# Optimization experiments

Hardware: AMD Instinct MI355X
Metric: run time of the kernel (lower is better)

Reference implementation:

```python
import jax, jax.numpy as jnp
import numpy as np

NUM_HEAD = 16


def setup_inputs() -> dict:
    key = jax.random.key(0)
    ks = jax.random.split(key, 4)
    B, C, D = 2, 2048, 1024
    hidden_states = jax.random.normal(ks[0], (B, C, D), dtype=jnp.float32)
    attention_mask = jnp.zeros((B, 1, C, C), dtype=jnp.float32)
    Wqkv = jax.random.normal(ks[1], (D, 3 * D), dtype=jnp.float32) * (D ** -0.5)
    bqkv = jnp.zeros((3 * D,), dtype=jnp.float32)
    Wo = jax.random.normal(ks[2], (D, D), dtype=jnp.float32) * (D ** -0.5)
    bo = jnp.zeros((D,), dtype=jnp.float32)
    return {"hidden_states": hidden_states, "attention_mask": attention_mask,
            "Wqkv": Wqkv, "bqkv": bqkv, "Wo": Wo, "bo": bo}


def reference(hidden_states, attention_mask, Wqkv, bqkv, Wo, bo):
    B, C, D = hidden_states.shape
    H = NUM_HEAD
    hd = D // H
    scaling = hd ** -0.5

    qkv = hidden_states @ Wqkv + bqkv                      # [B, C, 3D]
    q, k, v = jnp.split(qkv, 3, axis=-1)
    # [B, C, H, hd] -> [B, H, C, hd]
    q = q.reshape(B, C, H, hd).transpose(0, 2, 1, 3)
    k = k.reshape(B, C, H, hd).transpose(0, 2, 1, 3)
    v = v.reshape(B, C, H, hd).transpose(0, 2, 1, 3)

    scores = jnp.einsum("bhqd,bhkd->bhqk", q, k) * scaling  # [B, H, C, C]
    causal = jnp.tril(jnp.ones((C, C), dtype=bool))[None, None]
    mask = jnp.where(causal, attention_mask, -jnp.inf)      # [B, 1, C, C]
    probs = jax.nn.softmax(scores + mask, axis=-1)
    out = jnp.einsum("bhqk,bhkd->bhqd", probs, v)           # [B, H, C, hd]
    out = out.transpose(0, 2, 1, 3).reshape(B, C, D)
    return out @ Wo + bo
```

## Files before the change

### kernel.cpp

```cpp
#include <hip/hip_runtime.h>
#include <hip/hip_bf16.h>
#include <cstdint>
#include <cstddef>

typedef __attribute__((ext_vector_type(8))) short short8;
typedef __attribute__((ext_vector_type(4))) float f32x4;
typedef unsigned short u16;
typedef unsigned int u32;

#define B_ 2
#define C_ 2048
#define D_ 1024
#define H_ 16
#define HD_ 64

static __device__ __forceinline__ u16 f2b(float f) {
  u32 x = __builtin_bit_cast(u32, f);
  x += 0x7FFFu + ((x >> 16) & 1u);
  return (u16)(x >> 16);
}

__global__ void k_convert(const float* __restrict__ in, u16* __restrict__ out, int n) {
  int i = (blockIdx.x * blockDim.x + threadIdx.x) * 4;
  const int stride = gridDim.x * blockDim.x * 4;
  for (; i < n; i += stride) {
    float4 v = *reinterpret_cast<const float4*>(in + i);
    ushort4 o;
    o.x = f2b(v.x); o.y = f2b(v.y); o.z = f2b(v.z); o.w = f2b(v.w);
    *reinterpret_cast<ushort4*>(out + i) = o;
  }
}

__global__ void k_tconv(const float* __restrict__ in, u16* __restrict__ out, int R, int Cc) {
  __shared__ float tile[64][65];
  const int tC = blockIdx.x * 64;
  const int tR = blockIdx.y * 64;
  const int t = threadIdx.x;
  const int r0 = t >> 4;
  const int c0 = (t & 15) * 4;
#pragma unroll
  for (int ii = 0; ii < 4; ++ii) {
    int r = ii * 16 + r0;
    float4 v = *reinterpret_cast<const float4*>(&in[(size_t)(tR + r) * Cc + tC + c0]);
    tile[r][c0] = v.x; tile[r][c0 + 1] = v.y; tile[r][c0 + 2] = v.z; tile[r][c0 + 3] = v.w;
  }
  __syncthreads();
#pragma unroll
  for (int ii = 0; ii < 4; ++ii) {
    int c = ii * 16 + r0;
    ushort4 o;
    o.x = f2b(tile[c0 + 0][c]);
    o.y = f2b(tile[c0 + 1][c]);
    o.z = f2b(tile[c0 + 2][c]);
    o.w = f2b(tile[c0 + 3][c]);
    *reinterpret_cast<ushort4*>(&out[(size_t)(tC + c) * R + tR + c0]) = o;
  }
}

__global__ void k_maskflags(const float* __restrict__ mask, u32* __restrict__ flags) {
  const int bid = blockIdx.x;
  const int kt = bid & 15, qt = (bid >> 4) & 31, b = bid >> 9;
  const int t = threadIdx.x;
  const float* base = mask + ((size_t)b * C_ + qt * 64) * C_ + kt * 128;
  const int row = t >> 2, c0 = (t & 3) * 32;
  int any = 0;
#pragma unroll
  for (int i = 0; i < 8; ++i) {
    float4 v = *reinterpret_cast<const float4*>(base + (size_t)row * C_ + c0 + i * 4);
    any |= (v.x != 0.f) | (v.y != 0.f) | (v.z != 0.f) | (v.w != 0.f);
  }
  __shared__ int sh[4];
  const unsigned long long bal = __ballot(any);
  if ((t & 63) == 0) sh[t >> 6] = (bal != 0ull);
  __syncthreads();
  if (t == 0) flags[bid] = (u32)(sh[0] | sh[1] | sh[2] | sh[3]);
}

#define GLL16(gptr, lptr) __builtin_amdgcn_global_load_lds( \
    (const __attribute__((address_space(1))) u32*)(gptr),   \
    (__attribute__((address_space(3))) u32*)(lptr), 16, 0, 0)

template<int EPI, int BM>
__global__ __launch_bounds__(256) void k_gemm(
    const u16* __restrict__ A, const u16* __restrict__ Bt,
    int M, int N, int K, const float* __restrict__ bias,
    u16* __restrict__ Cq, u16* __restrict__ Ck, u16* __restrict__ Cv,
    float* __restrict__ Cf)
{
  constexpr int WCW = (BM == 128) ? 64 : 32;
  constexpr int NF = WCW / 16;
  __shared__ __align__(16) u16 As[BM * 64];
  __shared__ __align__(16) u16 Bs[128 * 64];
  const int t = threadIdx.x;
  const int l = t & 63, w = t >> 6;
  const int wr = (BM == 128) ? (w >> 1) : 0;
  const int wc = (BM == 128) ? (w & 1) : w;
  const int lr = l & 15, lg = l >> 4;
  const int swk = lr & 7;
  const int m0 = blockIdx.y * BM, n0 = blockIdx.x * 128;
  f32x4 acc[4][NF] = {};

  for (int k0 = 0; k0 < K; k0 += 64) {
#pragma unroll
    for (int s = 0; s < BM / 32; ++s) {
      const int u = s * 256 + t;
      const int row = u >> 3, slot = (u & 7) ^ (row & 7);
      GLL16(A + (size_t)(m0 + row) * K + k0 + (slot << 3), As + (u << 3));
    }
#pragma unroll
    for (int s = 0; s < 4; ++s) {
      const int u = s * 256 + t;
      const int row = u >> 3, slot = (u & 7) ^ (row & 7);
      GLL16(Bt + (size_t)(n0 + row) * K + k0 + (slot << 3), Bs + (u << 3));
    }
    __syncthreads();
    short8 af[2][4], bfr[2][NF];
#pragma unroll
    for (int s = 0; s < 2; ++s) {
#pragma unroll
      for (int m = 0; m < 4; ++m)
        af[s][m] = *reinterpret_cast<const short8*>(
            &As[((wr * 64 + m * 16 + lr) << 6) + (((s * 4 + lg) ^ swk) << 3)]);
#pragma unroll
      for (int n = 0; n < NF; ++n)
        bfr[s][n] = *reinterpret_cast<const short8*>(
            &Bs[((wc * WCW + n * 16 + lr) << 6) + (((s * 4 + lg) ^ swk) << 3)]);
    }
#pragma unroll
    for (int s = 0; s < 2; ++s)
#pragma unroll
      for (int m = 0; m < 4; ++m)
#pragma unroll
        for (int n = 0; n < NF; ++n)
          acc[m][n] = __builtin_amdgcn_mfma_f32_16x16x32_bf16(af[s][m], bfr[s][n], acc[m][n], 0, 0, 0);
    __syncthreads();
  }

#pragma unroll
  for (int m = 0; m < 4; ++m) {
    const int mg = m0 + wr * 64 + m * 16 + lg * 4;
    const int bq = mg >> 11, c0 = mg & 2047;
#pragma unroll
    for (int n = 0; n < NF; ++n) {
      const int ng = n0 + wc * WCW + n * 16 + lr;
      const float bia = bias[ng];
      if (EPI == 0) {
        const int reg = ng >> 10, d = ng & 1023, h = d >> 6, e = d & 63;
        if (reg == 2) {
          u16* vp = Cv + (((size_t)(bq * H_ + h) * HD_ + e) << 11) + c0;
#pragma unroll
          for (int j = 0; j < 4; ++j) vp[j] = f2b(acc[m][n][j] + bia);
        } else {
          u16* dst = (reg == 0) ? Cq : Ck;
#pragma unroll
          for (int j = 0; j < 4; ++j)
            dst[(((size_t)(bq * H_ + h) * C_ + c0 + j) << 6) + e] = f2b(acc[m][n][j] + bia);
        }
      } else {
#pragma unroll
        for (int j = 0; j < 4; ++j)
          Cf[(size_t)(mg + j) * N + ng] = acc[m][n][j] + bia;
      }
    }
  }
}

static __device__ __forceinline__ void stage_kv(
    const u16* __restrict__ Kbh, const u16* __restrict__ Vbh,
    u16* Kd, u16* Vd, int kt, int t)
{
#pragma unroll
  for (int ch = 0; ch < 4; ++ch) {
    const int u = ch * 256 + t;
    const int krow = u >> 3, kslot = (u & 7) ^ (krow & 7);
    GLL16(Kbh + (((size_t)(kt * 128 + krow)) << 6) + (kslot << 3), Kd + (u << 3));
    const int vrow = u >> 4, vslot = (u & 15) ^ (vrow & 7);
    GLL16(Vbh + (((size_t)vrow) << 11) + kt * 128 + (vslot << 3), Vd + (u << 3));
  }
}

__global__ __launch_bounds__(256) void k_attn(
    const u16* __restrict__ Q, const u16* __restrict__ Kb, const u16* __restrict__ Vt,
    const float* __restrict__ mask, const u32* __restrict__ flags, u16* __restrict__ O)
{
  __shared__ __align__(16) u16 Kl[2][128 * 64];
  __shared__ __align__(16) u16 Vl[2][64 * 128];
  __shared__ __align__(16) u16 Pl[4][16 * 128];
  const int bid = blockIdx.x;
  const int bh = bid & 31;
  const int pair = bid >> 5;
  const int b = bh >> 4, h = bh & 15;
  const int t = threadIdx.x;
  const int l = t & 63, w = t >> 6;
  const int lr = l & 15, lg = l >> 4;
  const int swk = lr & 7;
  const float scaling = 0.125f;

  const u16* Kbh = Kb + (size_t)bh * C_ * HD_;
  const u16* Vbh = Vt + (size_t)bh * HD_ * C_;
  u16* Pw = Pl[w];

#pragma unroll 1
  for (int phase = 0; phase < 2; ++phase) {
    const int qt = phase ? (31 - pair) : pair;
    const int ktmax = qt >> 1;
    const int qrb = qt * 64 + w * 16 + lg * 4;

    short8 aq[2];
    {
      const int qrow = qt * 64 + w * 16 + lr;
      const u16* qp = Q + ((size_t)bh * C_ + qrow) * HD_ + lg * 8;
      aq[0] = *reinterpret_cast<const short8*>(qp);
      aq[1] = *reinterpret_cast<const short8*>(qp + 32);
    }
    float mrun[4], srun[4];
    f32x4 oacc[4] = {};
#pragma unroll
    for (int j = 0; j < 4; ++j) { mrun[j] = -INFINITY; srun[j] = 0.f; }
    const float* mbase = mask + ((size_t)b * C_ + qrb) * C_ + lr;
    const u32* fbase = flags + ((b << 5) + qt) * 16;

    __builtin_amdgcn_s_barrier();
    stage_kv(Kbh, Vbh, Kl[0], Vl[0], 0, t);

    for (int kt = 0; kt <= ktmax; ++kt) {
      const int cur = kt & 1;
      asm volatile("s_waitcnt vmcnt(0)" ::: "memory");
      __builtin_amdgcn_s_barrier();

      const u32 mflag = fbase[kt];

      f32x4 sf[8] = {};
      __builtin_amdgcn_s_setprio(1);
#pragma unroll
      for (int s = 0; s < 2; ++s)
#pragma unroll
        for (int nf = 0; nf < 8; ++nf) {
          const short8 bk = *reinterpret_cast<const short8*>(
              &Kl[cur][((nf * 16 + lr) << 6) + (((s * 4 + lg) ^ swk) << 3)]);
          sf[nf] = __builtin_amdgcn_mfma_f32_16x16x32_bf16(aq[s], bk, sf[nf], 0, 0, 0);
        }
      __builtin_amdgcn_s_setprio(0);

      if (kt < ktmax) stage_kv(Kbh, Vbh, Kl[cur ^ 1], Vl[cur ^ 1], kt + 1, t);

      if (mflag) {
#pragma unroll
        for (int nf = 0; nf < 8; ++nf)
#pragma unroll
          for (int j = 0; j < 4; ++j)
            sf[nf][j] = fmaf(sf[nf][j], scaling, mbase[(size_t)j * C_ + kt * 128 + nf * 16]);
      } else {
#pragma unroll
        for (int nf = 0; nf < 8; ++nf)
#pragma unroll
          for (int j = 0; j < 4; ++j)
            sf[nf][j] *= scaling;
      }
      if (kt == ktmax) {
#pragma unroll
        for (int nf = 0; nf < 8; ++nf) {
          const int key = kt * 128 + nf * 16 + lr;
#pragma unroll
          for (int j = 0; j < 4; ++j)
            if (key > qrb + j) sf[nf][j] = -INFINITY;
        }
      }

      float pm[4] = {-INFINITY, -INFINITY, -INFINITY, -INFINITY};
#pragma unroll
      for (int nf = 0; nf < 8; ++nf)
#pragma unroll
        for (int j = 0; j < 4; ++j) pm[j] = fmaxf(pm[j], sf[nf][j]);
#pragma unroll
      for (int j = 0; j < 4; ++j) {
        pm[j] = fmaxf(pm[j], __shfl_xor(pm[j], 1));
        pm[j] = fmaxf(pm[j], __shfl_xor(pm[j], 2));
        pm[j] = fmaxf(pm[j], __shfl_xor(pm[j], 4));
        pm[j] = fmaxf(pm[j], __shfl_xor(pm[j], 8));
      }
#pragma unroll
      for (int j = 0; j < 4; ++j) {
        const float mn = fmaxf(mrun[j], pm[j]);
        const float rescale = __expf(mrun[j] - mn);
        float rsum = 0.f;
#pragma unroll
        for (int nf = 0; nf < 8; ++nf) {
          const float e = __expf(sf[nf][j] - mn);
          sf[nf][j] = e;
          rsum += e;
        }
        rsum += __shfl_xor(rsum, 1);
        rsum += __shfl_xor(rsum, 2);
        rsum += __shfl_xor(rsum, 4);
        rsum += __shfl_xor(rsum, 8);
        srun[j] = srun[j] * rescale + rsum;
        mrun[j] = mn;
#pragma unroll
        for (int df = 0; df < 4; ++df) oacc[df][j] *= rescale;
      }

#pragma unroll
      for (int j = 0; j < 4; ++j) {
        const int prow = lg * 4 + j;
        const int psw = (prow & 7) << 3;
#pragma unroll
        for (int nf = 0; nf < 8; ++nf)
          Pw[(prow << 7) + ((nf * 16 + lr) ^ psw)] = f2b(sf[nf][j]);
      }

      __builtin_amdgcn_s_setprio(1);
#pragma unroll
      for (int s2 = 0; s2 < 4; ++s2) {
        const short8 ap = *reinterpret_cast<const short8*>(
            &Pw[(lr << 7) + (((s2 * 4 + lg) ^ swk) << 3)]);
#pragma unroll
        for (int df = 0; df < 4; ++df) {
          const short8 bv = *reinterpret_cast<const short8*>(
              &Vl[cur][((df * 16 + lr) << 7) + (((s2 * 4 + lg) ^ swk) << 3)]);
          oacc[df] = __builtin_amdgcn_mfma_f32_16x16x32_bf16(ap, bv, oacc[df], 0, 0, 0);
        }
      }
      __builtin_amdgcn_s_setprio(0);
    }

    float rinv[4];
#pragma unroll
    for (int j = 0; j < 4; ++j) rinv[j] = 1.f / srun[j];
#pragma unroll
    for (int df = 0; df < 4; ++df) {
      const int dcol = df * 16 + lr;
#pragma unroll
      for (int j = 0; j < 4; ++j)
        O[((size_t)b * C_ + qrb + j) * D_ + h * HD_ + dcol] = f2b(oacc[df][j] * rinv[j]);
    }
  }
}

extern "C" void kernel_launch(void* const* d_in, const int* in_sizes, int n_in,
                              void* d_out, int out_size, void* d_ws, size_t ws_size,
                              hipStream_t stream) {
  const float* hs   = (const float*)d_in[0];
  const float* mask = (const float*)d_in[1];
  const float* Wqkv = (const float*)d_in[2];
  const float* bqkv = (const float*)d_in[3];
  const float* Wo   = (const float*)d_in[4];
  const float* bo   = (const float*)d_in[5];
  float* out = (float*)d_out;
  char* ws = (char*)d_ws;

  u16* hsb   = (u16*)(ws);
  u16* Wqkvt = (u16*)(ws + (8  << 20));
  u16* Wot   = (u16*)(ws + (14 << 20));
  u16* Qb    = (u16*)(ws + (16 << 20));
  u16* Kb    = (u16*)(ws + (24 << 20));
  u32* flags = (u32*)(ws + (32 << 20));
  u16* Vtb   = (u16*)(ws + (40 << 20));
  u16* AOb   = (u16*)(ws + (48 << 20));

  k_convert<<<2048, 256, 0, stream>>>(hs, hsb, 4096 * 1024);
  k_tconv<<<dim3(3072 / 64, 1024 / 64), 256, 0, stream>>>(Wqkv, Wqkvt, 1024, 3072);
  k_tconv<<<dim3(1024 / 64, 1024 / 64), 256, 0, stream>>>(Wo, Wot, 1024, 1024);
  k_maskflags<<<1024, 256, 0, stream>>>(mask, flags);
  k_gemm<0, 128><<<dim3(24, 32), 256, 0, stream>>>(hsb, Wqkvt, 4096, 3072, 1024, bqkv,
                                                   Qb, Kb, Vtb, nullptr);
  k_attn<<<512, 256, 0, stream>>>(Qb, Kb, Vtb, mask, flags, AOb);
  k_gemm<1, 64><<<dim3(8, 64), 256, 0, stream>>>(AOb, Wot, 4096, 1024, 1024, bo,
                                                 nullptr, nullptr, nullptr, out);
}
```

Measured before the change: 154.0 us.

## Rewrite attention with 32x32x16 MFMA, 128-row query tiles and 64-key blocks

The attention kernel now gives each wave 32 query rows and computes S^T = K·Q^T and O^T with 32x32x16 bf16 MFMAs over 64-key tiles. This lets row softmax reductions use one cross-half shuffle instead of four. Q is prescaled by 1/8 on load, P is packed with v_cvt_pk_bf16_f32, and the output is staged through LDS for coalesced 16-byte stores. Mask flags are recomputed at 64x64 granularity to match the new tiling. The grid shrinks to 256 blocks, which reduces parallelism, and prescaling Q in bf16 adds extra rounding.

```diff
diff --git a/kernel.cpp b/kernel.cpp
--- a/kernel.cpp
+++ b/kernel.cpp
@@ -5,6 +5,7 @@
 
 typedef __attribute__((ext_vector_type(8))) short short8;
 typedef __attribute__((ext_vector_type(4))) float f32x4;
+typedef __attribute__((ext_vector_type(16))) float f32x16;
 typedef unsigned short u16;
 typedef unsigned int u32;
 
@@ -59,13 +60,13 @@
 
 __global__ void k_maskflags(const float* __restrict__ mask, u32* __restrict__ flags) {
   const int bid = blockIdx.x;
-  const int kt = bid & 15, qt = (bid >> 4) & 31, b = bid >> 9;
+  const int kt = bid & 31, qs = (bid >> 5) & 31, b = bid >> 10;
   const int t = threadIdx.x;
-  const float* base = mask + ((size_t)b * C_ + qt * 64) * C_ + kt * 128;
-  const int row = t >> 2, c0 = (t & 3) * 32;
+  const float* base = mask + ((size_t)b * C_ + qs * 64) * C_ + kt * 64;
+  const int row = t >> 2, c0 = (t & 3) * 16;
   int any = 0;
 #pragma unroll
-  for (int i = 0; i < 8; ++i) {
+  for (int i = 0; i < 4; ++i) {
     float4 v = *reinterpret_cast<const float4*>(base + (size_t)row * C_ + c0 + i * 4);
     any |= (v.x != 0.f) | (v.y != 0.f) | (v.z != 0.f) | (v.w != 0.f);
   }
@@ -170,12 +171,11 @@
     u16* Kd, u16* Vd, int kt, int t)
 {
 #pragma unroll
-  for (int ch = 0; ch < 4; ++ch) {
+  for (int ch = 0; ch < 2; ++ch) {
     const int u = ch * 256 + t;
-    const int krow = u >> 3, kslot = (u & 7) ^ (krow & 7);
-    GLL16(Kbh + (((size_t)(kt * 128 + krow)) << 6) + (kslot << 3), Kd + (u << 3));
-    const int vrow = u >> 4, vslot = (u & 15) ^ (vrow & 7);
-    GLL16(Vbh + (((size_t)vrow) << 11) + kt * 128 + (vslot << 3), Vd + (u << 3));
+    const int row = u >> 3, slot = (u & 7) ^ (row & 7);
+    GLL16(Kbh + (((size_t)(kt * 64 + row)) << 6) + (slot << 3), Kd + (u << 3));
+    GLL16(Vbh + (((size_t)row) << 11) + kt * 64 + (slot << 3), Vd + (u << 3));
   }
 }
 
@@ -183,156 +183,155 @@
     const u16* __restrict__ Q, const u16* __restrict__ Kb, const u16* __restrict__ Vt,
     const float* __restrict__ mask, const u32* __restrict__ flags, u16* __restrict__ O)
 {
-  __shared__ __align__(16) u16 Kl[2][128 * 64];
-  __shared__ __align__(16) u16 Vl[2][64 * 128];
-  __shared__ __align__(16) u16 Pl[4][16 * 128];
+  __shared__ __align__(16) u16 Kl[2][64 * 64];
+  __shared__ __align__(16) u16 Vl[2][64 * 64];
+  __shared__ __align__(16) u16 Sc[4][2304];
   const int bid = blockIdx.x;
   const int bh = bid & 31;
-  const int pair = bid >> 5;
+  const int pr = bid >> 5;
   const int b = bh >> 4, h = bh & 15;
   const int t = threadIdx.x;
   const int l = t & 63, w = t >> 6;
-  const int lr = l & 15, lg = l >> 4;
-  const int swk = lr & 7;
-  const float scaling = 0.125f;
-
-  const u16* Kbh = Kb + (size_t)bh * C_ * HD_;
-  const u16* Vbh = Vt + (size_t)bh * HD_ * C_;
-  u16* Pw = Pl[w];
+  const int q = l & 31, hi = l >> 5;
+  const int q7 = q & 7;
+
+  const u16* Kbh = Kb + (size_t)bh * (C_ * HD_);
+  const u16* Vbh = Vt + (size_t)bh * (HD_ * C_);
+  char* Swb = reinterpret_cast<char*>(Sc[w]);
 
 #pragma unroll 1
   for (int phase = 0; phase < 2; ++phase) {
-    const int qt = phase ? (31 - pair) : pair;
-    const int ktmax = qt >> 1;
-    const int qrb = qt * 64 + w * 16 + lg * 4;
-
-    short8 aq[2];
+    const int qt = phase ? (15 - pr) : pr;
+    const int ktb = 2 * qt + 2;
+    const int q0w = qt * 128 + w * 32;
+    const int qg = q0w + q;
+    const int qmaxw = q0w + 31;
+
+    short8 aq[4];
     {
-      const int qrow = qt * 64 + w * 16 + lr;
-      const u16* qp = Q + ((size_t)bh * C_ + qrow) * HD_ + lg * 8;
-      aq[0] = *reinterpret_cast<const short8*>(qp);
-      aq[1] = *reinterpret_cast<const short8*>(qp + 32);
-    }
-    float mrun[4], srun[4];
-    f32x4 oacc[4] = {};
-#pragma unroll
-    for (int j = 0; j < 4; ++j) { mrun[j] = -INFINITY; srun[j] = 0.f; }
-    const float* mbase = mask + ((size_t)b * C_ + qrb) * C_ + lr;
-    const u32* fbase = flags + ((b << 5) + qt) * 16;
-
-    __builtin_amdgcn_s_barrier();
+      const u16* qp = Q + ((size_t)bh * C_ + qg) * HD_ + hi * 8;
+#pragma unroll
+      for (int kh = 0; kh < 4; ++kh) {
+        short8 v = *reinterpret_cast<const short8*>(qp + kh * 16);
+#pragma unroll
+        for (int i = 0; i < 8; ++i) {
+          const float f = __builtin_bit_cast(float, (u32)((u16)v[i]) << 16) * 0.125f;
+          v[i] = (short)f2b(f);
+        }
+        aq[kh] = v;
+      }
+    }
+
+    f32x16 oa0 = {}, oa1 = {};
+    float mrun = -INFINITY, srun = 0.f;
+    const float* mrow = mask + ((size_t)b * C_ + qg) * C_;
+    const u32* fb = flags + (size_t)(b * 32 + (q0w >> 6)) * 32;
+
     stage_kv(Kbh, Vbh, Kl[0], Vl[0], 0, t);
 
-    for (int kt = 0; kt <= ktmax; ++kt) {
+#pragma unroll 1
+    for (int kt = 0; kt < ktb; ++kt) {
       const int cur = kt & 1;
-      asm volatile("s_waitcnt vmcnt(0)" ::: "memory");
-      __builtin_amdgcn_s_barrier();
-
-      const u32 mflag = fbase[kt];
-
-      f32x4 sf[8] = {};
-      __builtin_amdgcn_s_setprio(1);
-#pragma unroll
-      for (int s = 0; s < 2; ++s)
-#pragma unroll
-        for (int nf = 0; nf < 8; ++nf) {
-          const short8 bk = *reinterpret_cast<const short8*>(
-              &Kl[cur][((nf * 16 + lr) << 6) + (((s * 4 + lg) ^ swk) << 3)]);
-          sf[nf] = __builtin_amdgcn_mfma_f32_16x16x32_bf16(aq[s], bk, sf[nf], 0, 0, 0);
-        }
-      __builtin_amdgcn_s_setprio(0);
-
-      if (kt < ktmax) stage_kv(Kbh, Vbh, Kl[cur ^ 1], Vl[cur ^ 1], kt + 1, t);
-
-      if (mflag) {
-#pragma unroll
-        for (int nf = 0; nf < 8; ++nf)
-#pragma unroll
-          for (int j = 0; j < 4; ++j)
-            sf[nf][j] = fmaf(sf[nf][j], scaling, mbase[(size_t)j * C_ + kt * 128 + nf * 16]);
-      } else {
-#pragma unroll
-        for (int nf = 0; nf < 8; ++nf)
-#pragma unroll
-          for (int j = 0; j < 4; ++j)
-            sf[nf][j] *= scaling;
-      }
-      if (kt == ktmax) {
-#pragma unroll
-        for (int nf = 0; nf < 8; ++nf) {
-          const int key = kt * 128 + nf * 16 + lr;
-#pragma unroll
-          for (int j = 0; j < 4; ++j)
-            if (key > qrb + j) sf[nf][j] = -INFINITY;
-        }
-      }
-
-      float pm[4] = {-INFINITY, -INFINITY, -INFINITY, -INFINITY};
-#pragma unroll
-      for (int nf = 0; nf < 8; ++nf)
-#pragma unroll
-        for (int j = 0; j < 4; ++j) pm[j] = fmaxf(pm[j], sf[nf][j]);
-#pragma unroll
-      for (int j = 0; j < 4; ++j) {
-        pm[j] = fmaxf(pm[j], __shfl_xor(pm[j], 1));
-        pm[j] = fmaxf(pm[j], __shfl_xor(pm[j], 2));
-        pm[j] = fmaxf(pm[j], __shfl_xor(pm[j], 4));
-        pm[j] = fmaxf(pm[j], __shfl_xor(pm[j], 8));
-      }
-#pragma unroll
-      for (int j = 0; j < 4; ++j) {
-        const float mn = fmaxf(mrun[j], pm[j]);
-        const float rescale = __expf(mrun[j] - mn);
-        float rsum = 0.f;
-#pragma unroll
-        for (int nf = 0; nf < 8; ++nf) {
-          const float e = __expf(sf[nf][j] - mn);
-          sf[nf][j] = e;
-          rsum += e;
-        }
-        rsum += __shfl_xor(rsum, 1);
-        rsum += __shfl_xor(rsum, 2);
-        rsum += __shfl_xor(rsum, 4);
-        rsum += __shfl_xor(rsum, 8);
-        srun[j] = srun[j] * rescale + rsum;
-        mrun[j] = mn;
-#pragma unroll
-        for (int df = 0; df < 4; ++df) oacc[df][j] *= rescale;
-      }
-
-#pragma unroll
-      for (int j = 0; j < 4; ++j) {
-        const int prow = lg * 4 + j;
-        const int psw = (prow & 7) << 3;
-#pragma unroll
-        for (int nf = 0; nf < 8; ++nf)
-          Pw[(prow << 7) + ((nf * 16 + lr) ^ psw)] = f2b(sf[nf][j]);
-      }
-
-      __builtin_amdgcn_s_setprio(1);
-#pragma unroll
-      for (int s2 = 0; s2 < 4; ++s2) {
-        const short8 ap = *reinterpret_cast<const short8*>(
-            &Pw[(lr << 7) + (((s2 * 4 + lg) ^ swk) << 3)]);
-#pragma unroll
-        for (int df = 0; df < 4; ++df) {
-          const short8 bv = *reinterpret_cast<const short8*>(
-              &Vl[cur][((df * 16 + lr) << 7) + (((s2 * 4 + lg) ^ swk) << 3)]);
-          oacc[df] = __builtin_amdgcn_mfma_f32_16x16x32_bf16(ap, bv, oacc[df], 0, 0, 0);
-        }
-      }
-      __builtin_amdgcn_s_setprio(0);
-    }
-
-    float rinv[4];
-#pragma unroll
-    for (int j = 0; j < 4; ++j) rinv[j] = 1.f / srun[j];
-#pragma unroll
-    for (int df = 0; df < 4; ++df) {
-      const int dcol = df * 16 + lr;
-#pragma unroll
-      for (int j = 0; j < 4; ++j)
-        O[((size_t)b * C_ + qrb + j) * D_ + h * HD_ + dcol] = f2b(oacc[df][j] * rinv[j]);
+      __syncthreads();
+      if (kt + 1 < ktb) stage_kv(Kbh, Vbh, Kl[cur ^ 1], Vl[cur ^ 1], kt + 1, t);
+      if (kt * 64 > qmaxw) continue;
+
+      const char* Kc = reinterpret_cast<const char*>(Kl[cur]);
+      const char* Vc = reinterpret_cast<const char*>(Vl[cur]);
+
+      f32x16 p0 = {}, p1 = {};
+#pragma unroll
+      for (int kh = 0; kh < 4; ++kh) {
+        const int sl = ((2 * kh + hi) ^ q7) << 4;
+        const short8 k0 = *reinterpret_cast<const short8*>(Kc + q * 128 + sl);
+        const short8 k1 = *reinterpret_cast<const short8*>(Kc + (32 + q) * 128 + sl);
+        p0 = __builtin_amdgcn_mfma_f32_32x32x16_bf16(k0, aq[kh], p0, 0, 0, 0);
+        p1 = __builtin_amdgcn_mfma_f32_32x32x16_bf16(k1, aq[kh], p1, 0, 0, 0);
+      }
+
+      if (fb[kt]) {
+        const float* mp = mrow + kt * 64 + 4 * hi;
+#pragma unroll
+        for (int g = 0; g < 4; ++g) {
+          const float4 m0 = *reinterpret_cast<const float4*>(mp + 8 * g);
+          const float4 m1 = *reinterpret_cast<const float4*>(mp + 32 + 8 * g);
+          p0[4*g+0] += m0.x; p0[4*g+1] += m0.y; p0[4*g+2] += m0.z; p0[4*g+3] += m0.w;
+          p1[4*g+0] += m1.x; p1[4*g+1] += m1.y; p1[4*g+2] += m1.z; p1[4*g+3] += m1.w;
+        }
+      }
+      if (kt * 64 + 63 > q0w) {
+#pragma unroll
+        for (int r = 0; r < 16; ++r) {
+          const int kl = kt * 64 + (r & 3) + 8 * (r >> 2) + 4 * hi;
+          if (kl > qg) p0[r] = -INFINITY;
+          if (kl + 32 > qg) p1[r] = -INFINITY;
+        }
+      }
+
+      float pm = -INFINITY;
+#pragma unroll
+      for (int r = 0; r < 16; ++r) pm = fmaxf(pm, fmaxf(p0[r], p1[r]));
+      pm = fmaxf(pm, __shfl_xor(pm, 32));
+      const float mn = fmaxf(fmaxf(mrun, pm), -1e30f);
+      const float rs = __expf(mrun - mn);
+      float sum = 0.f;
+#pragma unroll
+      for (int r = 0; r < 16; ++r) {
+        p0[r] = __expf(p0[r] - mn); sum += p0[r];
+        p1[r] = __expf(p1[r] - mn); sum += p1[r];
+      }
+      sum += __shfl_xor(sum, 32);
+      srun = srun * rs + sum;
+      mrun = mn;
+      oa0 *= rs; oa1 *= rs;
+
+#pragma unroll
+      for (int g = 0; g < 4; ++g) {
+#pragma unroll
+        for (int m = 0; m < 2; ++m) {
+          u32 w0, w1;
+          asm("v_cvt_pk_bf16_f32 %0, %1, %2" : "=v"(w0) : "v"(p0[4*g+2*m]), "v"(p0[4*g+2*m+1]));
+          asm("v_cvt_pk_bf16_f32 %0, %1, %2" : "=v"(w1) : "v"(p1[4*g+2*m]), "v"(p1[4*g+2*m+1]));
+          *reinterpret_cast<u32*>(Swb + q * 128 + ((g ^ q7) << 4) + 8 * hi + 4 * m) = w0;
+          *reinterpret_cast<u32*>(Swb + q * 128 + (((4 + g) ^ q7) << 4) + 8 * hi + 4 * m) = w1;
+        }
+      }
+      asm volatile("" ::: "memory");
+
+#pragma unroll
+      for (int ks = 0; ks < 4; ++ks) {
+        const int sl = ((2 * ks + hi) ^ q7) << 4;
+        const short8 bp = *reinterpret_cast<const short8*>(Swb + q * 128 + sl);
+        const short8 v0 = *reinterpret_cast<const short8*>(Vc + q * 128 + sl);
+        const short8 v1 = *reinterpret_cast<const short8*>(Vc + (32 + q) * 128 + sl);
+        oa0 = __builtin_amdgcn_mfma_f32_32x32x16_bf16(v0, bp, oa0, 0, 0, 0);
+        oa1 = __builtin_amdgcn_mfma_f32_32x32x16_bf16(v1, bp, oa1, 0, 0, 0);
+      }
+    }
+
+    const float rinv = 1.f / srun;
+#pragma unroll
+    for (int g = 0; g < 4; ++g) {
+      const int d0 = 8 * g + 4 * hi;
+      const float a0 = oa0[4*g+0] * rinv, a1 = oa0[4*g+1] * rinv;
+      const float a2 = oa0[4*g+2] * rinv, a3 = oa0[4*g+3] * rinv;
+      const float b0 = oa1[4*g+0] * rinv, b1 = oa1[4*g+1] * rinv;
+      const float b2 = oa1[4*g+2] * rinv, b3 = oa1[4*g+3] * rinv;
+      u32 w0, w1, w2, w3;
+      asm("v_cvt_pk_bf16_f32 %0, %1, %2" : "=v"(w0) : "v"(a0), "v"(a1));
+      asm("v_cvt_pk_bf16_f32 %0, %1, %2" : "=v"(w1) : "v"(a2), "v"(a3));
+      asm("v_cvt_pk_bf16_f32 %0, %1, %2" : "=v"(w2) : "v"(b0), "v"(b1));
+      asm("v_cvt_pk_bf16_f32 %0, %1, %2" : "=v"(w3) : "v"(b2), "v"(b3));
+      *reinterpret_cast<uint2*>(Swb + q * 144 + d0 * 2) = make_uint2(w0, w1);
+      *reinterpret_cast<uint2*>(Swb + q * 144 + (d0 + 32) * 2) = make_uint2(w2, w3);
+    }
+    asm volatile("" ::: "memory");
+    const int q2 = l >> 1, hf = l & 1;
+    u16* orow = O + ((size_t)b * C_ + q0w + q2) * D_ + h * 64 + hf * 32;
+#pragma unroll
+    for (int i = 0; i < 4; ++i) {
+      const short8 v = *reinterpret_cast<const short8*>(Swb + q2 * 144 + hf * 64 + i * 16);
+      *reinterpret_cast<short8*>(orow + i * 8) = v;
     }
   }
 }
@@ -361,10 +360,10 @@
   k_convert<<<2048, 256, 0, stream>>>(hs, hsb, 4096 * 1024);
   k_tconv<<<dim3(3072 / 64, 1024 / 64), 256, 0, stream>>>(Wqkv, Wqkvt, 1024, 3072);
   k_tconv<<<dim3(1024 / 64, 1024 / 64), 256, 0, stream>>>(Wo, Wot, 1024, 1024);
-  k_maskflags<<<1024, 256, 0, stream>>>(mask, flags);
+  k_maskflags<<<2048, 256, 0, stream>>>(mask, flags);
   k_gemm<0, 128><<<dim3(24, 32), 256, 0, stream>>>(hsb, Wqkvt, 4096, 3072, 1024, bqkv,
                                                    Qb, Kb, Vtb, nullptr);
-  k_attn<<<512, 256, 0, stream>>>(Qb, Kb, Vtb, mask, flags, AOb);
+  k_attn<<<256, 256, 0, stream>>>(Qb, Kb, Vtb, mask, flags, AOb);
   k_gemm<1, 64><<<dim3(8, 64), 256, 0, stream>>>(AOb, Wot, 4096, 1024, 1024, bo,
                                                  nullptr, nullptr, nullptr, out);
 }
```

Result: faster. 137.7 us (-10.6%).
